# Kernel tuning notes

Measured on AMD Instinct MI355X. Metric: run time of the kernel, lower is better.

## Reference

```python
import jax, jax.numpy as jnp
import numpy as np

NEG_MASK = -1.0e9  # matches torch masked_fill value


def setup_inputs() -> dict:
    key = jax.random.key(0)
    k1, k2, k3 = jax.random.split(key, 3)
    B, L, H, D = 4, 2048, 16, 64
    queries = jax.random.normal(k1, (B, L, H, D), dtype=jnp.float32)
    keys = jax.random.normal(k2, (B, L, H, D), dtype=jnp.float32)
    values = jax.random.normal(k3, (B, L, H, D), dtype=jnp.float32)
    return {"queries": queries, "keys": keys, "values": values}


def reference(queries, keys, values):
    # queries/keys/values: [B, L, H, D]
    B, L_q, H, D = queries.shape
    L_k = keys.shape[1]
    scale = 1.0 / jnp.sqrt(jnp.float32(D))
    # scores: [B, H, L_q, L_k]
    scores = jnp.einsum("blhd,bshd->bhls", queries, keys)
    # causal mask: allow s <= l (tril), fill disallowed with -1e9 BEFORE scaling,
    # exactly as the torch module does (masked_fill then softmax(scale*scores)).
    causal = jnp.tril(jnp.ones((L_q, L_k), dtype=bool))  # [L_q, L_k]
    scores = jnp.where(causal[None, None, :, :], scores, NEG_MASK)
    attn = jax.nn.softmax(scale * scores, axis=-1)  # dropout p=0.0 -> identity
    out = jnp.einsum("bhls,bshd->blhd", attn, values)
    return out
```

## Files before the change

### kernel.cpp

```cpp
#include <hip/hip_runtime.h>

typedef __attribute__((ext_vector_type(8))) short bf16x8;
typedef __attribute__((ext_vector_type(8))) unsigned short u16x8;
typedef __attribute__((ext_vector_type(4))) unsigned short u16x4;
typedef __attribute__((ext_vector_type(4))) float f32x4;
typedef __attribute__((ext_vector_type(16))) float f32x16;

#define MFMA32 __builtin_amdgcn_mfma_f32_32x32x16_bf16
#define MFMA16 __builtin_amdgcn_mfma_f32_16x16x32_bf16

constexpr int Bc = 4, Lc = 2048, Hc = 16, Dc = 64;
constexpr float SCL = 0.18033688011112042f;

__device__ __forceinline__ unsigned short f2bf(float f) {
  unsigned u = __float_as_uint(f);
  u += 0x7fff + ((u >> 16) & 1);
  return (unsigned short)(u >> 16);
}

__device__ __forceinline__ float fexp2(float x) {
  return __builtin_amdgcn_exp2f(x);
}

__device__ __forceinline__ unsigned cvtpk(float a, float b) {
  unsigned r;
  asm("v_cvt_pk_bf16_f32 %0, %1, %2" : "=v"(r) : "v"(a), "v"(b));
  return r;
}

__device__ __forceinline__ void glds16(const char* g, char* l) {
  __builtin_amdgcn_global_load_lds(
      (const __attribute__((address_space(1))) unsigned*)g,
      (__attribute__((address_space(3))) unsigned*)l, 16, 0, 0);
}

__global__ __launch_bounds__(256)
void prep18_kernel(const float* __restrict__ Kg, const float* __restrict__ Vg,
                   char* __restrict__ KB, char* __restrict__ VB) {
  __shared__ __align__(16) short vt[64 * 80];

  const int bid = blockIdx.x;
  const int bh = bid & 63;
  const int t  = bid >> 6;
  const int b  = bh >> 4;
  const int h  = bh & 15;

  const int tid = threadIdx.x;
  const int r   = tid >> 2;
  const int seg = (tid & 3) * 16;

  const size_t srow = ((size_t)((b * Lc + t * 64 + r) * Hc + h)) * Dc + seg;
  char* ktile = KB + (size_t)(bh * 32 + t) * 8192;
  char* vtile = VB + (size_t)(bh * 32 + t) * 8192;

  {
    const float* kp = Kg + srow;
    float4 c0 = *reinterpret_cast<const float4*>(kp + 0);
    float4 c1 = *reinterpret_cast<const float4*>(kp + 4);
    float4 c2 = *reinterpret_cast<const float4*>(kp + 8);
    float4 c3 = *reinterpret_cast<const float4*>(kp + 12);
    union { unsigned u[4]; u16x8 v; } w0, w1;
    w0.u[0] = cvtpk(c0.x, c0.y); w0.u[1] = cvtpk(c0.z, c0.w);
    w0.u[2] = cvtpk(c1.x, c1.y); w0.u[3] = cvtpk(c1.z, c1.w);
    w1.u[0] = cvtpk(c2.x, c2.y); w1.u[1] = cvtpk(c2.z, c2.w);
    w1.u[2] = cvtpk(c3.x, c3.y); w1.u[3] = cvtpk(c3.z, c3.w);
    const int kc   = seg >> 4;
    const int kt2  = r >> 5;
    const int lane = r & 31;
    *reinterpret_cast<u16x8*>(ktile + ((kt2 * 4 + kc) * 64 + lane) * 16) = w0.v;
    *reinterpret_cast<u16x8*>(ktile + ((kt2 * 4 + kc) * 64 + lane + 32) * 16) = w1.v;
  }

  {
    const float* vp = Vg + srow;
    float4 v0 = *reinterpret_cast<const float4*>(vp + 0);
    float4 v1 = *reinterpret_cast<const float4*>(vp + 4);
    float4 v2 = *reinterpret_cast<const float4*>(vp + 8);
    float4 v3 = *reinterpret_cast<const float4*>(vp + 12);
    float vv[16];
    vv[0] = v0.x; vv[1] = v0.y; vv[2] = v0.z; vv[3] = v0.w;
    vv[4] = v1.x; vv[5] = v1.y; vv[6] = v1.z; vv[7] = v1.w;
    vv[8] = v2.x; vv[9] = v2.y; vv[10] = v2.z; vv[11] = v2.w;
    vv[12] = v3.x; vv[13] = v3.y; vv[14] = v3.z; vv[15] = v3.w;
#pragma unroll
    for (int j = 0; j < 16; ++j)
      vt[(seg + j) * 80 + r] = (short)f2bf(vv[j]);
  }
  __syncthreads();

  {
    const int d    = tid >> 2;
    const int kseg = (tid & 3) * 16;
    u16x4 p0 = *reinterpret_cast<const u16x4*>(vt + d * 80 + kseg + 0);
    u16x4 p1 = *reinterpret_cast<const u16x4*>(vt + d * 80 + kseg + 4);
    u16x4 p2 = *reinterpret_cast<const u16x4*>(vt + d * 80 + kseg + 8);
    u16x4 p3 = *reinterpret_cast<const u16x4*>(vt + d * 80 + kseg + 12);
    u16x8 a0, a1;
    a0[0] = p0[0]; a0[1] = p0[1]; a0[2] = p0[2]; a0[3] = p0[3];
    a0[4] = p2[0]; a0[5] = p2[1]; a0[6] = p2[2]; a0[7] = p2[3];
    a1[0] = p1[0]; a1[1] = p1[1]; a1[2] = p1[2]; a1[3] = p1[3];
    a1[4] = p3[0]; a1[5] = p3[1]; a1[6] = p3[2]; a1[7] = p3[3];
    const int dt2  = d >> 5;
    const int kc   = kseg >> 4;
    const int lane = d & 31;
    *reinterpret_cast<u16x8*>(vtile + ((dt2 * 4 + kc) * 64 + lane) * 16) = a0;
    *reinterpret_cast<u16x8*>(vtile + ((dt2 * 4 + kc) * 64 + lane + 32) * 16) = a1;
  }
}

__global__ __launch_bounds__(512)
void fattn18_kernel(const float* __restrict__ Qg, const char* __restrict__ KB,
                    const char* __restrict__ VB, float* __restrict__ Og) {
  __shared__ __align__(128) char smem[32768];

  const int p    = blockIdx.x;
  const int head = p & 63;
  const int qt   = (p < 256) ? (7 - (p >> 6)) : ((p >> 6) - 4);
  const int b    = head >> 4;
  const int h    = head & 15;

  const int tid = threadIdx.x;
  const int w   = tid >> 6;
  const int l   = tid & 63;
  const int q5  = l & 31;
  const int hp  = l >> 5;

  const int qrow = qt * 256 + w * 32 + q5;
  const int qmin = qt * 256 + w * 32;
  const int qmax = qmin + 31;

  bf16x8 qf[4];
  {
    const float* qp = Qg + ((size_t)((b * Lc + qrow) * Hc + h)) * Dc;
#pragma unroll
    for (int kc = 0; kc < 4; ++kc) {
      const int d0 = kc * 16 + hp * 8;
      float4 a = *reinterpret_cast<const float4*>(qp + d0);
      float4 bb = *reinterpret_cast<const float4*>(qp + d0 + 4);
      union { unsigned u[4]; bf16x8 v; } f;
      f.u[0] = cvtpk(a.x * SCL, a.y * SCL);
      f.u[1] = cvtpk(a.z * SCL, a.w * SCL);
      f.u[2] = cvtpk(bb.x * SCL, bb.y * SCL);
      f.u[3] = cvtpk(bb.z * SCL, bb.w * SCL);
      qf[kc] = f.v;
    }
  }

  f32x16 o0, o1;
#pragma unroll
  for (int i = 0; i < 16; ++i) { o0[i] = 0.f; o1[i] = 0.f; }
  float m_run = -3.0e38f, l_run = 0.0f;

  const char* kbase = KB + ((size_t)head * 32) * 8192;
  const char* vbase = VB + ((size_t)head * 32) * 8192;
  const int to = tid * 16;
  const int wl = w * 1024;

  auto stage = [&](int bufi, int kt) {
    const char* kb = kbase + (size_t)kt * 8192;
    const char* vb = vbase + (size_t)kt * 8192;
    char* dK = smem + bufi * 16384;
    char* dV = dK + 8192;
    glds16(kb + to, dK + wl);
    glds16(vb + to, dV + wl);
  };

  const int nkt = 4 * qt + 4;
  int buf = 0;
  stage(0, 0);

  for (int kt = 0; kt < nkt; ++kt) {
    if (kt + 1 < nkt) {
      stage(buf ^ 1, kt + 1);
      asm volatile("s_waitcnt vmcnt(2)" ::: "memory");
    } else {
      asm volatile("s_waitcnt vmcnt(0)" ::: "memory");
    }
    __builtin_amdgcn_s_barrier();

    const int kv0 = kt * 64;
    if (kv0 <= qmax) {
      const char* smK = smem + buf * 16384;
      const char* smV = smK + 8192;

      f32x16 s0, s1;
#pragma unroll
      for (int i = 0; i < 16; ++i) { s0[i] = 0.f; s1[i] = 0.f; }
#pragma unroll
      for (int kc = 0; kc < 4; ++kc) {
        bf16x8 k0 = *reinterpret_cast<const bf16x8*>(smK + (0 * 4 + kc) * 1024 + l * 16);
        bf16x8 k1 = *reinterpret_cast<const bf16x8*>(smK + (1 * 4 + kc) * 1024 + l * 16);
        s0 = MFMA32(k0, qf[kc], s0, 0, 0, 0);
        s1 = MFMA32(k1, qf[kc], s1, 0, 0, 0);
      }

      float pv[32];
#pragma unroll
      for (int g = 0; g < 16; ++g) { pv[g] = s0[g]; pv[16 + g] = s1[g]; }

      if (kv0 + 63 > qmin) {
#pragma unroll
        for (int g = 0; g < 32; ++g) {
          const int k = (g & 3) + 8 * ((g >> 2) & 3) + 4 * hp + 32 * (g >> 4);
          if (kv0 + k > qrow) pv[g] = -3.0e38f;
        }
      }

      float vmax = pv[0];
#pragma unroll
      for (int g = 1; g < 32; ++g) vmax = fmaxf(vmax, pv[g]);
      vmax = fmaxf(vmax, __shfl_xor(vmax, 32));
      if (!__all(vmax <= m_run + 8.0f)) {
        const float m_new = fmaxf(m_run, vmax);
        const float alpha = fexp2(m_run - m_new);
        l_run *= alpha;
        m_run = m_new;
#pragma unroll
        for (int i = 0; i < 16; ++i) { o0[i] *= alpha; o1[i] *= alpha; }
      }

      float rsum = 0.f;
#pragma unroll
      for (int g = 0; g < 32; ++g) { pv[g] = fexp2(pv[g] - m_run); rsum += pv[g]; }
      l_run += rsum;

      bf16x8 pf[4];
#pragma unroll
      for (int kc = 0; kc < 4; ++kc) {
        const int G = 8 * kc;
        union { unsigned u[4]; bf16x8 v; } f;
        f.u[0] = cvtpk(pv[G + 0], pv[G + 1]);
        f.u[1] = cvtpk(pv[G + 2], pv[G + 3]);
        f.u[2] = cvtpk(pv[G + 4], pv[G + 5]);
        f.u[3] = cvtpk(pv[G + 6], pv[G + 7]);
        pf[kc] = f.v;
      }

#pragma unroll
      for (int kc = 0; kc < 4; ++kc) {
        bf16x8 v0 = *reinterpret_cast<const bf16x8*>(smV + (0 * 4 + kc) * 1024 + l * 16);
        bf16x8 v1 = *reinterpret_cast<const bf16x8*>(smV + (1 * 4 + kc) * 1024 + l * 16);
        o0 = MFMA32(v0, pf[kc], o0, 0, 0, 0);
        o1 = MFMA32(v1, pf[kc], o1, 0, 0, 0);
      }
    }

    __syncthreads();
    buf ^= 1;
  }

  const float l_tot = l_run + __shfl_xor(l_run, 32);
  const float inv = 1.0f / l_tot;
  float* op = Og + ((size_t)((b * Lc + qrow) * Hc + h)) * Dc;
#pragma unroll
  for (int rq = 0; rq < 4; ++rq) {
    float4 st0, st1;
    st0.x = o0[4 * rq + 0] * inv; st0.y = o0[4 * rq + 1] * inv;
    st0.z = o0[4 * rq + 2] * inv; st0.w = o0[4 * rq + 3] * inv;
    st1.x = o1[4 * rq + 0] * inv; st1.y = o1[4 * rq + 1] * inv;
    st1.z = o1[4 * rq + 2] * inv; st1.w = o1[4 * rq + 3] * inv;
    *reinterpret_cast<float4*>(op + 8 * rq + 4 * hp) = st0;
    *reinterpret_cast<float4*>(op + 32 + 8 * rq + 4 * hp) = st1;
  }
}

__global__ __launch_bounds__(256)
void fattn_fallback(const float* __restrict__ Qg, const float* __restrict__ Kg,
                    const float* __restrict__ Vg, float* __restrict__ Og) {
  __shared__ __align__(128) char smem[32768];
  char* smK = smem;
  char* smV = smem + 16384;

  const int bid  = blockIdx.x;
  const int head = bid >> 5;
  const int qt   = bid & 31;
  const int b    = head >> 4;
  const int h    = head & 15;
  const int q0   = qt * 64;

  const int tid = threadIdx.x;
  const int w   = tid >> 6;
  const int l   = tid & 63;
  const int lo  = l & 15;
  const int hi4 = l >> 4;

  const int qrow = q0 + w * 16 + lo;
  const float* qp = Qg + ((size_t)((b * Lc + qrow) * Hc + h)) * Dc;
  bf16x8 qf[2];
#pragma unroll
  for (int dc = 0; dc < 2; ++dc) {
    float4 a = *reinterpret_cast<const float4*>(qp + dc * 32 + hi4 * 8);
    float4 c = *reinterpret_cast<const float4*>(qp + dc * 32 + hi4 * 8 + 4);
    bf16x8 f;
    f[0] = (short)f2bf(a.x * SCL); f[1] = (short)f2bf(a.y * SCL);
    f[2] = (short)f2bf(a.z * SCL); f[3] = (short)f2bf(a.w * SCL);
    f[4] = (short)f2bf(c.x * SCL); f[5] = (short)f2bf(c.y * SCL);
    f[6] = (short)f2bf(c.z * SCL); f[7] = (short)f2bf(c.w * SCL);
    qf[dc] = f;
  }

  f32x4 o[4];
#pragma unroll
  for (int dt = 0; dt < 4; ++dt) { o[dt][0] = 0.f; o[dt][1] = 0.f; o[dt][2] = 0.f; o[dt][3] = 0.f; }
  float m_run = -3.0e38f, l_run = 0.0f;

  const int sk   = tid >> 2;
  const int sd   = (tid & 3) * 16;
  const int swzK = (sk & 7) << 4;
  const int swzA = (lo & 7) << 4;

  const int nkt = qt + 1;
  for (int kt = 0; kt < nkt; ++kt) {
    const int kv0 = kt * 64;
    __syncthreads();
    {
      const float* kpr = Kg + ((size_t)((b * Lc + kv0 + sk) * Hc + h)) * Dc + sd;
      float4 c0 = *reinterpret_cast<const float4*>(kpr + 0);
      float4 c1 = *reinterpret_cast<const float4*>(kpr + 4);
      float4 c2 = *reinterpret_cast<const float4*>(kpr + 8);
      float4 c3 = *reinterpret_cast<const float4*>(kpr + 12);
      u16x8 w0, w1;
      w0[0] = f2bf(c0.x); w0[1] = f2bf(c0.y); w0[2] = f2bf(c0.z); w0[3] = f2bf(c0.w);
      w0[4] = f2bf(c1.x); w0[5] = f2bf(c1.y); w0[6] = f2bf(c1.z); w0[7] = f2bf(c1.w);
      w1[0] = f2bf(c2.x); w1[1] = f2bf(c2.y); w1[2] = f2bf(c2.z); w1[3] = f2bf(c2.w);
      w1[4] = f2bf(c3.x); w1[5] = f2bf(c3.y); w1[6] = f2bf(c3.z); w1[7] = f2bf(c3.w);
      *reinterpret_cast<u16x8*>(smK + sk * 128 + ((sd * 2) ^ swzK)) = w0;
      *reinterpret_cast<u16x8*>(smK + sk * 128 + ((sd * 2 + 16) ^ swzK)) = w1;

      const float* vpr = Vg + ((size_t)((b * Lc + kv0 + sk) * Hc + h)) * Dc + sd;
      float4 v0 = *reinterpret_cast<const float4*>(vpr + 0);
      float4 v1 = *reinterpret_cast<const float4*>(vpr + 4);
      float4 v2 = *reinterpret_cast<const float4*>(vpr + 8);
      float4 v3 = *reinterpret_cast<const float4*>(vpr + 12);
      float vv[16];
      vv[0] = v0.x; vv[1] = v0.y; vv[2] = v0.z; vv[3] = v0.w;
      vv[4] = v1.x; vv[5] = v1.y; vv[6] = v1.z; vv[7] = v1.w;
      vv[8] = v2.x; vv[9] = v2.y; vv[10] = v2.z; vv[11] = v2.w;
      vv[12] = v3.x; vv[13] = v3.y; vv[14] = v3.z; vv[15] = v3.w;
#pragma unroll
      for (int j = 0; j < 16; ++j) {
        const int d = sd + j;
        *reinterpret_cast<unsigned short*>(smV + d * 128 + ((sk * 2) ^ ((j & 7) << 4))) = f2bf(vv[j]);
      }
    }
    __syncthreads();

    f32x4 s[4];
#pragma unroll
    for (int ks = 0; ks < 4; ++ks) {
      const int rb = (ks * 16 + lo) * 128;
      bf16x8 a0 = *reinterpret_cast<const bf16x8*>(smK + rb + ((hi4 * 16) ^ swzA));
      bf16x8 a1 = *reinterpret_cast<const bf16x8*>(smK + rb + ((64 + hi4 * 16) ^ swzA));
      f32x4 c; c[0] = 0.f; c[1] = 0.f; c[2] = 0.f; c[3] = 0.f;
      c = MFMA16(a0, qf[0], c, 0, 0, 0);
      c = MFMA16(a1, qf[1], c, 0, 0, 0);
      s[ks] = c;
    }

    const bool diag = (kt == nkt - 1);
    float vmax = -3.0e38f;
#pragma unroll
    for (int ks = 0; ks < 4; ++ks) {
#pragma unroll
      for (int i = 0; i < 4; ++i) {
        float x = s[ks][i];
        if (diag) {
          const int kg = kv0 + ks * 16 + hi4 * 4 + i;
          if (kg > qrow) x = -3.0e38f;
        }
        s[ks][i] = x;
        vmax = fmaxf(vmax, x);
      }
    }
    vmax = fmaxf(vmax, __shfl_xor(vmax, 16));
    vmax = fmaxf(vmax, __shfl_xor(vmax, 32));
    const float m_new = fmaxf(m_run, vmax);
    const float alpha = fexp2(m_run - m_new);

    float rsum = 0.f;
    unsigned pk2[4][2];
#pragma unroll
    for (int ks = 0; ks < 4; ++ks) {
      const float p0 = fexp2(s[ks][0] - m_new);
      const float p1 = fexp2(s[ks][1] - m_new);
      const float p2 = fexp2(s[ks][2] - m_new);
      const float p3 = fexp2(s[ks][3] - m_new);
      rsum += (p0 + p1) + (p2 + p3);
      pk2[ks][0] = (unsigned)f2bf(p0) | ((unsigned)f2bf(p1) << 16);
      pk2[ks][1] = (unsigned)f2bf(p2) | ((unsigned)f2bf(p3) << 16);
    }
    rsum += __shfl_xor(rsum, 16);
    rsum += __shfl_xor(rsum, 32);
    l_run = l_run * alpha + rsum;
    m_run = m_new;
#pragma unroll
    for (int dt = 0; dt < 4; ++dt) {
      o[dt][0] *= alpha; o[dt][1] *= alpha; o[dt][2] *= alpha; o[dt][3] *= alpha;
    }

    const int srcA = lo + ((l & 16) << 1);
    const int srcB = srcA + 16;
    const bool up = (l & 32) != 0;
    bf16x8 pf[2];
#pragma unroll
    for (int c2 = 0; c2 < 2; ++c2) {
      const unsigned A0x = (unsigned)__shfl((int)pk2[2 * c2][0], srcA);
      const unsigned A0y = (unsigned)__shfl((int)pk2[2 * c2][1], srcA);
      const unsigned A1x = (unsigned)__shfl((int)pk2[2 * c2][0], srcB);
      const unsigned A1y = (unsigned)__shfl((int)pk2[2 * c2][1], srcB);
      const unsigned B0x = (unsigned)__shfl((int)pk2[2 * c2 + 1][0], srcA);
      const unsigned B0y = (unsigned)__shfl((int)pk2[2 * c2 + 1][1], srcA);
      const unsigned B1x = (unsigned)__shfl((int)pk2[2 * c2 + 1][0], srcB);
      const unsigned B1y = (unsigned)__shfl((int)pk2[2 * c2 + 1][1], srcB);
      union { unsigned u[4]; bf16x8 v; } cvt;
      cvt.u[0] = up ? B0x : A0x;
      cvt.u[1] = up ? B0y : A0y;
      cvt.u[2] = up ? B1x : A1x;
      cvt.u[3] = up ? B1y : A1y;
      pf[c2] = cvt.v;
    }

#pragma unroll
    for (int dt = 0; dt < 4; ++dt) {
      const int rb = (dt * 16 + lo) * 128;
#pragma unroll
      for (int c2 = 0; c2 < 2; ++c2) {
        bf16x8 vf = *reinterpret_cast<const bf16x8*>(smV + rb + ((c2 * 64 + hi4 * 16) ^ swzA));
        o[dt] = MFMA16(vf, pf[c2], o[dt], 0, 0, 0);
      }
    }
  }

  const float inv = 1.0f / l_run;
  float* op = Og + ((size_t)((b * Lc + qrow) * Hc + h)) * Dc;
#pragma unroll
  for (int dt = 0; dt < 4; ++dt) {
    float4 st;
    st.x = o[dt][0] * inv; st.y = o[dt][1] * inv;
    st.z = o[dt][2] * inv; st.w = o[dt][3] * inv;
    *reinterpret_cast<float4*>(op + dt * 16 + hi4 * 4) = st;
  }
}

extern "C" void kernel_launch(void* const* d_in, const int* in_sizes, int n_in,
                              void* d_out, int out_size, void* d_ws, size_t ws_size,
                              hipStream_t stream) {
  const float* Qg = (const float*)d_in[0];
  const float* Kg = (const float*)d_in[1];
  const float* Vg = (const float*)d_in[2];
  float* Og = (float*)d_out;

  const size_t blob_bytes = (size_t)64 * 32 * 8192;
  if (ws_size >= 2 * blob_bytes) {
    char* KB = (char*)d_ws;
    char* VB = KB + blob_bytes;
    hipLaunchKernelGGL(prep18_kernel, dim3(2048), dim3(256), 0, stream, Kg, Vg, KB, VB);
    hipLaunchKernelGGL(fattn18_kernel, dim3(512), dim3(512), 0, stream, Qg, KB, VB, Og);
  } else {
    hipLaunchKernelGGL(fattn_fallback, dim3(2048), dim3(256), 0, stream, Qg, Kg, Vg, Og);
  }
}
```

Before: 73.87 us.

## Split causal attention KV range across two blocks and combine partials

Adds a split-K flash attention path that launches 1024 blocks, each handling half of the causal KV range for a 256-row query tile, writing unnormalized partial outputs plus running max and sum to workspace. A separate combine kernel merges the two halves with log-sum-exp rescaling. The aim is more parallelism and better load balance across CUs than the 512-block single-pass kernel. In exchange it adds an extra launch and writes and rereads about 64 MB of fp32 partials, and it only runs if the workspace is large enough.

```diff
diff --git a/kernel.cpp b/kernel.cpp
--- a/kernel.cpp
+++ b/kernel.cpp
@@ -35,7 +35,7 @@
 }
 
 __global__ __launch_bounds__(256)
-void prep18_kernel(const float* __restrict__ Kg, const float* __restrict__ Vg,
+void prep19_kernel(const float* __restrict__ Kg, const float* __restrict__ Vg,
                    char* __restrict__ KB, char* __restrict__ VB) {
   __shared__ __align__(16) short vt[64 * 80];
 
@@ -109,6 +109,207 @@
 }
 
 __global__ __launch_bounds__(512)
+void fattn_sk_kernel(const float* __restrict__ Qg, const char* __restrict__ KB,
+                     const char* __restrict__ VB, float* __restrict__ OP0,
+                     float* __restrict__ OP1, float* __restrict__ ML0,
+                     float* __restrict__ ML1) {
+  __shared__ __align__(128) char smem[32768];
+
+  const int p    = blockIdx.x;
+  const int head = p & 63;
+  const int idx  = (p >> 6) & 7;
+  const int half = p >> 9;
+  const int qt   = (idx < 4) ? (7 - idx) : (idx - 4);
+  const int b    = head >> 4;
+  const int h    = head & 15;
+
+  float* __restrict__ OP = half ? OP1 : OP0;
+  float* __restrict__ ML = half ? ML1 : ML0;
+
+  const int tid = threadIdx.x;
+  const int w   = tid >> 6;
+  const int l   = tid & 63;
+  const int q5  = l & 31;
+  const int hp  = l >> 5;
+
+  const int qrow = qt * 256 + w * 32 + q5;
+  const int qmin = qt * 256 + w * 32;
+  const int qmax = qmin + 31;
+
+  bf16x8 qf[4];
+  {
+    const float* qp = Qg + ((size_t)((b * Lc + qrow) * Hc + h)) * Dc;
+#pragma unroll
+    for (int kc = 0; kc < 4; ++kc) {
+      const int d0 = kc * 16 + hp * 8;
+      float4 a = *reinterpret_cast<const float4*>(qp + d0);
+      float4 bb = *reinterpret_cast<const float4*>(qp + d0 + 4);
+      union { unsigned u[4]; bf16x8 v; } f;
+      f.u[0] = cvtpk(a.x * SCL, a.y * SCL);
+      f.u[1] = cvtpk(a.z * SCL, a.w * SCL);
+      f.u[2] = cvtpk(bb.x * SCL, bb.y * SCL);
+      f.u[3] = cvtpk(bb.z * SCL, bb.w * SCL);
+      qf[kc] = f.v;
+    }
+  }
+
+  f32x16 o0, o1;
+#pragma unroll
+  for (int i = 0; i < 16; ++i) { o0[i] = 0.f; o1[i] = 0.f; }
+  float m_run = -3.0e38f, l_run = 0.0f;
+
+  const char* kbase = KB + ((size_t)head * 32) * 8192;
+  const char* vbase = VB + ((size_t)head * 32) * 8192;
+  const int to = tid * 16;
+  const int wl = w * 1024;
+
+  auto stage = [&](int bufi, int kt) {
+    const char* kb = kbase + (size_t)kt * 8192;
+    const char* vb = vbase + (size_t)kt * 8192;
+    char* dK = smem + bufi * 16384;
+    char* dV = dK + 8192;
+    glds16(kb + to, dK + wl);
+    glds16(vb + to, dV + wl);
+  };
+
+  const int kt0 = half ? (2 * qt + 2) : 0;
+  const int kt1 = half ? (4 * qt + 4) : (2 * qt + 2);
+  int buf = 0;
+  stage(0, kt0);
+
+  for (int kt = kt0; kt < kt1; ++kt) {
+    if (kt + 1 < kt1) {
+      stage(buf ^ 1, kt + 1);
+      asm volatile("s_waitcnt vmcnt(2)" ::: "memory");
+    } else {
+      asm volatile("s_waitcnt vmcnt(0)" ::: "memory");
+    }
+    __builtin_amdgcn_s_barrier();
+
+    const int kv0 = kt * 64;
+    if (kv0 <= qmax) {
+      const char* smK = smem + buf * 16384;
+      const char* smV = smK + 8192;
+
+      f32x16 s0, s1;
+#pragma unroll
+      for (int i = 0; i < 16; ++i) { s0[i] = 0.f; s1[i] = 0.f; }
+#pragma unroll
+      for (int kc = 0; kc < 4; ++kc) {
+        bf16x8 k0 = *reinterpret_cast<const bf16x8*>(smK + (0 * 4 + kc) * 1024 + l * 16);
+        bf16x8 k1 = *reinterpret_cast<const bf16x8*>(smK + (1 * 4 + kc) * 1024 + l * 16);
+        s0 = MFMA32(k0, qf[kc], s0, 0, 0, 0);
+        s1 = MFMA32(k1, qf[kc], s1, 0, 0, 0);
+      }
+
+      float pv[32];
+#pragma unroll
+      for (int g = 0; g < 16; ++g) { pv[g] = s0[g]; pv[16 + g] = s1[g]; }
+
+      if (kv0 + 63 > qmin) {
+#pragma unroll
+        for (int g = 0; g < 32; ++g) {
+          const int k = (g & 3) + 8 * ((g >> 2) & 3) + 4 * hp + 32 * (g >> 4);
+          if (kv0 + k > qrow) pv[g] = -3.0e38f;
+        }
+      }
+
+      float vmax = pv[0];
+#pragma unroll
+      for (int g = 1; g < 32; ++g) vmax = fmaxf(vmax, pv[g]);
+      vmax = fmaxf(vmax, __shfl_xor(vmax, 32));
+      if (!__all(vmax <= m_run + 8.0f)) {
+        const float m_new = fmaxf(m_run, vmax);
+        const float alpha = fexp2(m_run - m_new);
+        l_run *= alpha;
+        m_run = m_new;
+#pragma unroll
+        for (int i = 0; i < 16; ++i) { o0[i] *= alpha; o1[i] *= alpha; }
+      }
+
+      float rsum = 0.f;
+#pragma unroll
+      for (int g = 0; g < 32; ++g) { pv[g] = fexp2(pv[g] - m_run); rsum += pv[g]; }
+      l_run += rsum;
+
+      bf16x8 pf[4];
+#pragma unroll
+      for (int kc = 0; kc < 4; ++kc) {
+        const int G = 8 * kc;
+        union { unsigned u[4]; bf16x8 v; } f;
+        f.u[0] = cvtpk(pv[G + 0], pv[G + 1]);
+        f.u[1] = cvtpk(pv[G + 2], pv[G + 3]);
+        f.u[2] = cvtpk(pv[G + 4], pv[G + 5]);
+        f.u[3] = cvtpk(pv[G + 6], pv[G + 7]);
+        pf[kc] = f.v;
+      }
+
+#pragma unroll
+      for (int kc = 0; kc < 4; ++kc) {
+        bf16x8 v0 = *reinterpret_cast<const bf16x8*>(smV + (0 * 4 + kc) * 1024 + l * 16);
+        bf16x8 v1 = *reinterpret_cast<const bf16x8*>(smV + (1 * 4 + kc) * 1024 + l * 16);
+        o0 = MFMA32(v0, pf[kc], o0, 0, 0, 0);
+        o1 = MFMA32(v1, pf[kc], o1, 0, 0, 0);
+      }
+    }
+
+    __syncthreads();
+    buf ^= 1;
+  }
+
+  const float l_tot = l_run + __shfl_xor(l_run, 32);
+  const int rid = (b * Lc + qrow) * Hc + h;
+  float* op = OP + (size_t)rid * 64;
+#pragma unroll
+  for (int rq = 0; rq < 4; ++rq) {
+    float4 st0, st1;
+    st0.x = o0[4 * rq + 0]; st0.y = o0[4 * rq + 1];
+    st0.z = o0[4 * rq + 2]; st0.w = o0[4 * rq + 3];
+    st1.x = o1[4 * rq + 0]; st1.y = o1[4 * rq + 1];
+    st1.z = o1[4 * rq + 2]; st1.w = o1[4 * rq + 3];
+    *reinterpret_cast<float4*>(op + 8 * rq + 4 * hp) = st0;
+    *reinterpret_cast<float4*>(op + 32 + 8 * rq + 4 * hp) = st1;
+  }
+  if (hp == 0) {
+    ML[(size_t)rid * 2 + 0] = m_run;
+    ML[(size_t)rid * 2 + 1] = l_tot;
+  }
+}
+
+__global__ __launch_bounds__(256)
+void combine_kernel(const float* __restrict__ OP0, const float* __restrict__ OP1,
+                    const float* __restrict__ ML0, const float* __restrict__ ML1,
+                    float* __restrict__ Og) {
+  const int gid = blockIdx.x * 256 + threadIdx.x;
+  const int rid = gid >> 2;
+  const int seg = (gid & 3) * 16;
+
+  const float m1 = ML0[(size_t)rid * 2 + 0];
+  const float l1 = ML0[(size_t)rid * 2 + 1];
+  const float m2 = ML1[(size_t)rid * 2 + 0];
+  const float l2 = ML1[(size_t)rid * 2 + 1];
+  const float m  = fmaxf(m1, m2);
+  const float s1 = fexp2(m1 - m);
+  const float s2 = fexp2(m2 - m);
+  const float inv = 1.0f / (l1 * s1 + l2 * s2);
+
+  const float* p1 = OP0 + (size_t)rid * 64 + seg;
+  const float* p2 = OP1 + (size_t)rid * 64 + seg;
+  float* po = Og + (size_t)rid * 64 + seg;
+#pragma unroll
+  for (int i = 0; i < 4; ++i) {
+    float4 a = *reinterpret_cast<const float4*>(p1 + 4 * i);
+    float4 c = *reinterpret_cast<const float4*>(p2 + 4 * i);
+    float4 r;
+    r.x = (a.x * s1 + c.x * s2) * inv;
+    r.y = (a.y * s1 + c.y * s2) * inv;
+    r.z = (a.z * s1 + c.z * s2) * inv;
+    r.w = (a.w * s1 + c.w * s2) * inv;
+    *reinterpret_cast<float4*>(po + 4 * i) = r;
+  }
+}
+
+__global__ __launch_bounds__(512)
 void fattn18_kernel(const float* __restrict__ Qg, const char* __restrict__ KB,
                     const char* __restrict__ VB, float* __restrict__ Og) {
   __shared__ __align__(128) char smem[32768];
@@ -451,10 +652,26 @@
   float* Og = (float*)d_out;
 
   const size_t blob_bytes = (size_t)64 * 32 * 8192;
-  if (ws_size >= 2 * blob_bytes) {
+  const size_t op_bytes   = (size_t)131072 * 64 * 4;
+  const size_t ml_bytes   = (size_t)131072 * 2 * 4;
+  const size_t sk_bytes   = 2 * blob_bytes + 2 * op_bytes + 2 * ml_bytes;
+
+  if (ws_size >= sk_bytes) {
+    char* KB  = (char*)d_ws;
+    char* VB  = KB + blob_bytes;
+    float* OP0 = (float*)(VB + blob_bytes);
+    float* OP1 = OP0 + (size_t)131072 * 64;
+    float* ML0 = OP1 + (size_t)131072 * 64;
+    float* ML1 = ML0 + (size_t)131072 * 2;
+    hipLaunchKernelGGL(prep19_kernel, dim3(2048), dim3(256), 0, stream, Kg, Vg, KB, VB);
+    hipLaunchKernelGGL(fattn_sk_kernel, dim3(1024), dim3(512), 0, stream,
+                       Qg, KB, VB, OP0, OP1, ML0, ML1);
+    hipLaunchKernelGGL(combine_kernel, dim3(2048), dim3(256), 0, stream,
+                       OP0, OP1, ML0, ML1, Og);
+  } else if (ws_size >= 2 * blob_bytes) {
     char* KB = (char*)d_ws;
     char* VB = KB + blob_bytes;
-    hipLaunchKernelGGL(prep18_kernel, dim3(2048), dim3(256), 0, stream, Kg, Vg, KB, VB);
+    hipLaunchKernelGGL(prep19_kernel, dim3(2048), dim3(256), 0, stream, Kg, Vg, KB, VB);
     hipLaunchKernelGGL(fattn18_kernel, dim3(512), dim3(512), 0, stream, Qg, KB, VB, Og);
   } else {
     hipLaunchKernelGGL(fattn_fallback, dim3(2048), dim3(256), 0, stream, Qg, Kg, Vg, Og);
```

Result: slower. 100.0 us (+35.4%).
